# Kernel tuning notes

Hardware: AMD Instinct MI355X
Metric: run time of the kernel (lower is better)

Reference implementation:

```python
import jax, jax.numpy as jnp
import numpy as np

B = 16384
IN_FEATURES = 256
OUT_FEATURES = 4096
CH_GROUP = 8
NUM_SLICE = IN_FEATURES // CH_GROUP  # 32


def setup_inputs() -> dict:
    key = jax.random.key(0)
    kx, kw = jax.random.split(key)
    x = jax.random.normal(kx, (B, IN_FEATURES), dtype=jnp.float32)
    # Stacked weights of the 32 tiny Linear(ch_group -> out_features, bias=False)
    # layers; W[i] corresponds to fc_i.weight with shape [out_features, ch_group].
    W = jax.random.normal(kw, (NUM_SLICE, OUT_FEATURES, CH_GROUP), dtype=jnp.float32) * (1.0 / np.sqrt(CH_GROUP))
    return {"x": x, "W": W}


def reference(x, W):
    # Equivalent to sum_i fc_i(x[:, i*cg:(i+1)*cg]) = fused block GEMM.
    xs = x.reshape(x.shape[0], NUM_SLICE, CH_GROUP)  # [B, S, C]
    # out[b,o] = sum_{s,c} xs[b,s,c] * W[s,o,c]
    return jnp.einsum('bsc,soc->bo', xs, W)
```

## Files before the change

kernel.cpp:

```cpp
#include <hip/hip_runtime.h>
#include <hip/hip_bf16.h>


typedef __attribute__((ext_vector_type(8)))  __bf16          bf16x8;
typedef __attribute__((ext_vector_type(8)))  unsigned short  ushort8;
typedef __attribute__((ext_vector_type(4)))  float           floatx4;

__device__ __forceinline__ unsigned short f2bf(float f) {
    union { float f; unsigned u; } v; v.f = f;
    unsigned r = v.u + 0x7fffu + ((v.u >> 16) & 1u);
    return (unsigned short)(r >> 16);
}

__global__ __launch_bounds__(256) void prep_kernel(
    const float* __restrict__ x, const float* __restrict__ W,
    unsigned short* __restrict__ xb, unsigned short* __restrict__ wb) {
    const int b = blockIdx.x;
    if (b < 2048) {
        const int t = b * 256 + threadIdx.x;
        const float4* p = (const float4*)x;
        float4 a = p[2 * t], c = p[2 * t + 1];
        ushort8 v;
        v[0] = f2bf(a.x); v[1] = f2bf(a.y); v[2] = f2bf(a.z); v[3] = f2bf(a.w);
        v[4] = f2bf(c.x); v[5] = f2bf(c.y); v[6] = f2bf(c.z); v[7] = f2bf(c.w);
        *(ushort8*)(xb + (size_t)t * 8) = v;
    } else {
        const int t = (b - 2048) * 256 + threadIdx.x;
        const int s = t >> 12;
        const int o = t & 4095;
        const float4* p = (const float4*)(W + (size_t)s * 32768 + (size_t)o * 8);
        float4 a = p[0], c = p[1];
        ushort8 v;
        v[0] = f2bf(a.x); v[1] = f2bf(a.y); v[2] = f2bf(a.z); v[3] = f2bf(a.w);
        v[4] = f2bf(c.x); v[5] = f2bf(c.y); v[6] = f2bf(c.z); v[7] = f2bf(c.w);
        *(ushort8*)(wb + (size_t)o * 256 + (size_t)s * 8) = v;
    }
}

__device__ __forceinline__ void gload_lds16(const unsigned short* g, unsigned short* l) {
    __builtin_amdgcn_global_load_lds(
        (const __attribute__((address_space(1))) unsigned int*)(const void*)g,
        (__attribute__((address_space(3))) unsigned int*)(void*)l,
        16, 0, 0);
}

__global__ __launch_bounds__(256, 4) void gemm_kernel(
    const unsigned short* __restrict__ A,
    const unsigned short* __restrict__ Bt,
    float* __restrict__ C) {
    __shared__ __align__(16) unsigned short lsA[2][128 * 32];
    __shared__ __align__(16) unsigned short lsB[2][128 * 32];

    const int tid  = threadIdx.x;
    const int wave = tid >> 6;
    const int lane = tid & 63;

    const int flat = blockIdx.y * 32 + blockIdx.x;
    const int nid  = (flat & 7) * 512 + (flat >> 3);
    const int bm   = nid >> 5;
    const int bn   = nid & 31;

    const int sr  = tid >> 2;
    const int gch = (tid & 3) ^ ((tid >> 3) & 3);
    const unsigned short* Ag = A  + ((size_t)(bm * 128 + sr)) * 256 + gch * 8;
    const unsigned short* Bg = Bt + ((size_t)(bn * 128 + sr)) * 256 + gch * 8;
    unsigned short* laW[2] = { &lsA[0][wave * 512], &lsA[1][wave * 512] };
    unsigned short* lbW[2] = { &lsB[0][wave * 512], &lsB[1][wave * 512] };

    const int wrow = wave >> 1, wcol = wave & 1;
    const int fr = lane & 15;
    const int fq = lane >> 4;
    const int so = (fq ^ ((fr >> 1) & 3)) * 8;
    const unsigned short* aF[2] = { &lsA[0][(wrow * 64 + fr) * 32] + so,
                                    &lsA[1][(wrow * 64 + fr) * 32] + so };
    const unsigned short* bF[2] = { &lsB[0][(wcol * 64 + fr) * 32] + so,
                                    &lsB[1][(wcol * 64 + fr) * 32] + so };

    floatx4 acc[4][4] = {};

    gload_lds16(Ag,            laW[0]);
    gload_lds16(Ag + 64 * 256, laW[0] + 2048);
    gload_lds16(Bg,            lbW[0]);
    gload_lds16(Bg + 64 * 256, lbW[0] + 2048);
    __syncthreads();

#pragma unroll
    for (int kt = 0; kt < 8; ++kt) {
        const int cur = kt & 1;
        if (kt < 7) {
            const int ko = (kt + 1) * 32;
            gload_lds16(Ag + ko,            laW[cur ^ 1]);
            gload_lds16(Ag + ko + 64 * 256, laW[cur ^ 1] + 2048);
            gload_lds16(Bg + ko,            lbW[cur ^ 1]);
            gload_lds16(Bg + ko + 64 * 256, lbW[cur ^ 1] + 2048);
        }

        bf16x8 af[4], bv[4];
#pragma unroll
        for (int i = 0; i < 4; ++i) {
            af[i] = *(const bf16x8*)(const void*)(aF[cur] + i * 512);
            bv[i] = *(const bf16x8*)(const void*)(bF[cur] + i * 512);
        }
#pragma unroll
        for (int j = 0; j < 4; ++j)
#pragma unroll
            for (int i = 0; i < 4; ++i)
                acc[j][i] = __builtin_amdgcn_mfma_f32_16x16x32_bf16(
                    bv[j], af[i], acc[j][i], 0, 0, 0);
        __syncthreads();
    }

    const int row0 = bm * 128 + wrow * 64 + fr;
    const int col0 = bn * 128 + wcol * 64 + fq * 4;
#pragma unroll
    for (int i = 0; i < 4; ++i) {
        float* Cp = C + (size_t)(row0 + i * 16) * 4096 + col0;
#pragma unroll
        for (int j = 0; j < 4; ++j)
            __builtin_nontemporal_store(acc[j][i], (floatx4*)(Cp + j * 16));
    }
}

extern "C" void kernel_launch(void* const* d_in, const int* in_sizes, int n_in,
                              void* d_out, int out_size, void* d_ws, size_t ws_size,
                              hipStream_t stream) {
    const float* x = (const float*)d_in[0];
    const float* W = (const float*)d_in[1];
    float* out = (float*)d_out;

    unsigned short* xb = (unsigned short*)d_ws;
    unsigned short* wb = xb + (size_t)16384 * 256;

    prep_kernel<<<2560, 256, 0, stream>>>(x, W, xb, wb);

    dim3 grid(32, 128);
    gemm_kernel<<<grid, 256, 0, stream>>>(xb, wb, out);
}
```

Baseline: 312.7 us.

## Fuse fp32-to-bf16 conversion into GEMM and drop separate prep kernel

New measurement: 352.8 us. 12.8% more time.

```diff
diff --git a/kernel.cpp b/kernel.cpp
--- a/kernel.cpp
+++ b/kernel.cpp
@@ -2,54 +2,16 @@
 #include <hip/hip_bf16.h>
 
 
-typedef __attribute__((ext_vector_type(8)))  __bf16          bf16x8;
-typedef __attribute__((ext_vector_type(8)))  unsigned short  ushort8;
-typedef __attribute__((ext_vector_type(4)))  float           floatx4;
+typedef __attribute__((ext_vector_type(8))) __bf16 bf16x8;
+typedef __attribute__((ext_vector_type(4))) __bf16 bf16x4;
+typedef __attribute__((ext_vector_type(4))) float  floatx4;
 
-__device__ __forceinline__ unsigned short f2bf(float f) {
-    union { float f; unsigned u; } v; v.f = f;
-    unsigned r = v.u + 0x7fffu + ((v.u >> 16) & 1u);
-    return (unsigned short)(r >> 16);
-}
-
-__global__ __launch_bounds__(256) void prep_kernel(
-    const float* __restrict__ x, const float* __restrict__ W,
-    unsigned short* __restrict__ xb, unsigned short* __restrict__ wb) {
-    const int b = blockIdx.x;
-    if (b < 2048) {
-        const int t = b * 256 + threadIdx.x;
-        const float4* p = (const float4*)x;
-        float4 a = p[2 * t], c = p[2 * t + 1];
-        ushort8 v;
-        v[0] = f2bf(a.x); v[1] = f2bf(a.y); v[2] = f2bf(a.z); v[3] = f2bf(a.w);
-        v[4] = f2bf(c.x); v[5] = f2bf(c.y); v[6] = f2bf(c.z); v[7] = f2bf(c.w);
-        *(ushort8*)(xb + (size_t)t * 8) = v;
-    } else {
-        const int t = (b - 2048) * 256 + threadIdx.x;
-        const int s = t >> 12;
-        const int o = t & 4095;
-        const float4* p = (const float4*)(W + (size_t)s * 32768 + (size_t)o * 8);
-        float4 a = p[0], c = p[1];
-        ushort8 v;
-        v[0] = f2bf(a.x); v[1] = f2bf(a.y); v[2] = f2bf(a.z); v[3] = f2bf(a.w);
-        v[4] = f2bf(c.x); v[5] = f2bf(c.y); v[6] = f2bf(c.z); v[7] = f2bf(c.w);
-        *(ushort8*)(wb + (size_t)o * 256 + (size_t)s * 8) = v;
-    }
-}
-
-__device__ __forceinline__ void gload_lds16(const unsigned short* g, unsigned short* l) {
-    __builtin_amdgcn_global_load_lds(
-        (const __attribute__((address_space(1))) unsigned int*)(const void*)g,
-        (__attribute__((address_space(3))) unsigned int*)(void*)l,
-        16, 0, 0);
-}
-
-__global__ __launch_bounds__(256, 4) void gemm_kernel(
-    const unsigned short* __restrict__ A,
-    const unsigned short* __restrict__ Bt,
+__global__ __launch_bounds__(256) void gemm_kernel(
+    const float* __restrict__ X,
+    const float* __restrict__ W,
     float* __restrict__ C) {
-    __shared__ __align__(16) unsigned short lsA[2][128 * 32];
-    __shared__ __align__(16) unsigned short lsB[2][128 * 32];
+    __shared__ __align__(16) __bf16 lsA[2][128 * 32];
+    __shared__ __align__(16) __bf16 lsB[2][128 * 32];
 
     const int tid  = threadIdx.x;
     const int wave = tid >> 6;
@@ -60,46 +22,58 @@
     const int bm   = nid >> 5;
     const int bn   = nid & 31;
 
-    const int sr  = tid >> 2;
-    const int gch = (tid & 3) ^ ((tid >> 3) & 3);
-    const unsigned short* Ag = A  + ((size_t)(bm * 128 + sr)) * 256 + gch * 8;
-    const unsigned short* Bg = Bt + ((size_t)(bn * 128 + sr)) * 256 + gch * 8;
-    unsigned short* laW[2] = { &lsA[0][wave * 512], &lsA[1][wave * 512] };
-    unsigned short* lbW[2] = { &lsB[0][wave * 512], &lsB[1][wave * 512] };
+    const int achunk = tid & 7;
+    const int arb    = tid >> 3;
+    const int akey   = (arb >> 1) & 3;
+    const float* Xa  = X + (size_t)(bm * 128 + arb) * 256 + achunk * 4;
+    const int adst   = arb * 32 + (((achunk >> 1) ^ akey) * 8) + (achunk & 1) * 4;
+
+    const int brb   = tid >> 1;
+    const int bhalf = tid & 1;
+    const int bkey  = (brb >> 1) & 3;
+    const float* Wb = W + (size_t)(bn * 128 + brb) * 8 + bhalf * 4;
+    const int bdst  = brb * 32 + bhalf * 4;
 
     const int wrow = wave >> 1, wcol = wave & 1;
     const int fr = lane & 15;
     const int fq = lane >> 4;
-    const int so = (fq ^ ((fr >> 1) & 3)) * 8;
-    const unsigned short* aF[2] = { &lsA[0][(wrow * 64 + fr) * 32] + so,
-                                    &lsA[1][(wrow * 64 + fr) * 32] + so };
-    const unsigned short* bF[2] = { &lsB[0][(wcol * 64 + fr) * 32] + so,
-                                    &lsB[1][(wcol * 64 + fr) * 32] + so };
+    const int fch  = (fq ^ ((fr >> 1) & 3)) * 8;
+    const int aoff = (wrow * 64 + fr) * 32 + fch;
+    const int boff = (wcol * 64 + fr) * 32 + fch;
 
+    floatx4 ra[2][4], rb[2][4];
     floatx4 acc[4][4] = {};
 
-    gload_lds16(Ag,            laW[0]);
-    gload_lds16(Ag + 64 * 256, laW[0] + 2048);
-    gload_lds16(Bg,            lbW[0]);
-    gload_lds16(Bg + 64 * 256, lbW[0] + 2048);
-    __syncthreads();
-
+    auto loadT = [&](int set, int kt) {
 #pragma unroll
-    for (int kt = 0; kt < 8; ++kt) {
-        const int cur = kt & 1;
-        if (kt < 7) {
-            const int ko = (kt + 1) * 32;
-            gload_lds16(Ag + ko,            laW[cur ^ 1]);
-            gload_lds16(Ag + ko + 64 * 256, laW[cur ^ 1] + 2048);
-            gload_lds16(Bg + ko,            lbW[cur ^ 1]);
-            gload_lds16(Bg + ko + 64 * 256, lbW[cur ^ 1] + 2048);
+        for (int q = 0; q < 4; ++q)
+            ra[set][q] = *(const floatx4*)(Xa + (size_t)q * 32 * 256 + kt * 32);
+#pragma unroll
+        for (int l = 0; l < 4; ++l)
+            rb[set][l] = *(const floatx4*)(Wb + (size_t)(kt * 4 + l) * 32768);
+    };
+    auto writeT = [&](int buf, int set) {
+#pragma unroll
+        for (int q = 0; q < 4; ++q) {
+            bf16x4 v;
+            v[0] = (__bf16)ra[set][q][0]; v[1] = (__bf16)ra[set][q][1];
+            v[2] = (__bf16)ra[set][q][2]; v[3] = (__bf16)ra[set][q][3];
+            *(bf16x4*)&lsA[buf][adst + q * 1024] = v;
         }
-
+#pragma unroll
+        for (int l = 0; l < 4; ++l) {
+            bf16x4 v;
+            v[0] = (__bf16)rb[set][l][0]; v[1] = (__bf16)rb[set][l][1];
+            v[2] = (__bf16)rb[set][l][2]; v[3] = (__bf16)rb[set][l][3];
+            *(bf16x4*)&lsB[buf][bdst + ((l ^ bkey) * 8)] = v;
+        }
+    };
+    auto compute = [&](int buf) {
         bf16x8 af[4], bv[4];
 #pragma unroll
         for (int i = 0; i < 4; ++i) {
-            af[i] = *(const bf16x8*)(const void*)(aF[cur] + i * 512);
-            bv[i] = *(const bf16x8*)(const void*)(bF[cur] + i * 512);
+            af[i] = *(const bf16x8*)&lsA[buf][aoff + i * 512];
+            bv[i] = *(const bf16x8*)&lsB[buf][boff + i * 512];
         }
 #pragma unroll
         for (int j = 0; j < 4; ++j)
@@ -107,7 +81,24 @@
             for (int i = 0; i < 4; ++i)
                 acc[j][i] = __builtin_amdgcn_mfma_f32_16x16x32_bf16(
                     bv[j], af[i], acc[j][i], 0, 0, 0);
-        __syncthreads();
+    };
+
+    loadT(0, 0);
+    writeT(0, 0);
+    loadT(1, 1);
+    asm volatile("s_waitcnt lgkmcnt(0)" ::: "memory");
+    __builtin_amdgcn_s_barrier();
+
+#pragma unroll
+    for (int kt = 0; kt < 8; ++kt) {
+        const int cur = kt & 1;
+        if (kt < 7) writeT(cur ^ 1, (kt + 1) & 1);
+        if (kt < 6) loadT(cur, kt + 2);
+        compute(cur);
+        if (kt < 7) {
+            asm volatile("s_waitcnt lgkmcnt(0)" ::: "memory");
+            __builtin_amdgcn_s_barrier();
+        }
     }
 
     const int row0 = bm * 128 + wrow * 64 + fr;
@@ -127,12 +118,8 @@
     const float* x = (const float*)d_in[0];
     const float* W = (const float*)d_in[1];
     float* out = (float*)d_out;
-
-    unsigned short* xb = (unsigned short*)d_ws;
-    unsigned short* wb = xb + (size_t)16384 * 256;
-
-    prep_kernel<<<2560, 256, 0, stream>>>(x, W, xb, wb);
+    (void)d_ws; (void)ws_size;
 
     dim3 grid(32, 128);
-    gemm_kernel<<<grid, 256, 0, stream>>>(xb, wb, out);
+    gemm_kernel<<<grid, 256, 0, stream>>>(x, W, out);
 }
```

## Triple-buffer LDS tiles with one barrier per k-step in GEMM

Applied to the files above, without the earlier changes.

After: 305.5 us. 1.02x faster.

```diff
diff --git a/kernel.cpp b/kernel.cpp
--- a/kernel.cpp
+++ b/kernel.cpp
@@ -44,12 +44,18 @@
         16, 0, 0);
 }
 
-__global__ __launch_bounds__(256, 4) void gemm_kernel(
+__device__ __forceinline__ void block_sync() {
+    asm volatile("" ::: "memory");
+    __builtin_amdgcn_s_barrier();
+    asm volatile("" ::: "memory");
+}
+
+__global__ __launch_bounds__(256, 3) void gemm_kernel(
     const unsigned short* __restrict__ A,
     const unsigned short* __restrict__ Bt,
     float* __restrict__ C) {
-    __shared__ __align__(16) unsigned short lsA[2][128 * 32];
-    __shared__ __align__(16) unsigned short lsB[2][128 * 32];
+    __shared__ __align__(16) unsigned short lsA[3][128 * 32];
+    __shared__ __align__(16) unsigned short lsB[3][128 * 32];
 
     const int tid  = threadIdx.x;
     const int wave = tid >> 6;
@@ -64,50 +70,53 @@
     const int gch = (tid & 3) ^ ((tid >> 3) & 3);
     const unsigned short* Ag = A  + ((size_t)(bm * 128 + sr)) * 256 + gch * 8;
     const unsigned short* Bg = Bt + ((size_t)(bn * 128 + sr)) * 256 + gch * 8;
-    unsigned short* laW[2] = { &lsA[0][wave * 512], &lsA[1][wave * 512] };
-    unsigned short* lbW[2] = { &lsB[0][wave * 512], &lsB[1][wave * 512] };
+    unsigned short* laW[3] = { &lsA[0][wave * 512], &lsA[1][wave * 512], &lsA[2][wave * 512] };
+    unsigned short* lbW[3] = { &lsB[0][wave * 512], &lsB[1][wave * 512], &lsB[2][wave * 512] };
 
     const int wrow = wave >> 1, wcol = wave & 1;
     const int fr = lane & 15;
     const int fq = lane >> 4;
     const int so = (fq ^ ((fr >> 1) & 3)) * 8;
-    const unsigned short* aF[2] = { &lsA[0][(wrow * 64 + fr) * 32] + so,
-                                    &lsA[1][(wrow * 64 + fr) * 32] + so };
-    const unsigned short* bF[2] = { &lsB[0][(wcol * 64 + fr) * 32] + so,
-                                    &lsB[1][(wcol * 64 + fr) * 32] + so };
+    const unsigned short* aF[3] = { &lsA[0][(wrow * 64 + fr) * 32] + so,
+                                    &lsA[1][(wrow * 64 + fr) * 32] + so,
+                                    &lsA[2][(wrow * 64 + fr) * 32] + so };
+    const unsigned short* bF[3] = { &lsB[0][(wcol * 64 + fr) * 32] + so,
+                                    &lsB[1][(wcol * 64 + fr) * 32] + so,
+                                    &lsB[2][(wcol * 64 + fr) * 32] + so };
 
     floatx4 acc[4][4] = {};
 
-    gload_lds16(Ag,            laW[0]);
-    gload_lds16(Ag + 64 * 256, laW[0] + 2048);
-    gload_lds16(Bg,            lbW[0]);
-    gload_lds16(Bg + 64 * 256, lbW[0] + 2048);
-    __syncthreads();
+    auto stage = [&](int b, int kt) {
+        const int ko = kt * 32;
+        gload_lds16(Ag + ko,            laW[b]);
+        gload_lds16(Ag + ko + 64 * 256, laW[b] + 2048);
+        gload_lds16(Bg + ko,            lbW[b]);
+        gload_lds16(Bg + ko + 64 * 256, lbW[b] + 2048);
+    };
+
+    stage(0, 0);
+    stage(1, 1);
 
 #pragma unroll
     for (int kt = 0; kt < 8; ++kt) {
-        const int cur = kt & 1;
-        if (kt < 7) {
-            const int ko = (kt + 1) * 32;
-            gload_lds16(Ag + ko,            laW[cur ^ 1]);
-            gload_lds16(Ag + ko + 64 * 256, laW[cur ^ 1] + 2048);
-            gload_lds16(Bg + ko,            lbW[cur ^ 1]);
-            gload_lds16(Bg + ko + 64 * 256, lbW[cur ^ 1] + 2048);
-        }
+        const int b = kt % 3;
+        if (kt < 7) asm volatile("s_waitcnt vmcnt(4)" ::: "memory");
+        else        asm volatile("s_waitcnt vmcnt(0)" ::: "memory");
+        block_sync();
 
         bf16x8 af[4], bv[4];
 #pragma unroll
         for (int i = 0; i < 4; ++i) {
-            af[i] = *(const bf16x8*)(const void*)(aF[cur] + i * 512);
-            bv[i] = *(const bf16x8*)(const void*)(bF[cur] + i * 512);
+            af[i] = *(const bf16x8*)(const void*)(aF[b] + i * 512);
+            bv[i] = *(const bf16x8*)(const void*)(bF[b] + i * 512);
         }
+        if (kt < 6) stage((kt + 2) % 3, kt + 2);
 #pragma unroll
         for (int j = 0; j < 4; ++j)
 #pragma unroll
             for (int i = 0; i < 4; ++i)
                 acc[j][i] = __builtin_amdgcn_mfma_f32_16x16x32_bf16(
                     bv[j], af[i], acc[j][i], 0, 0, 0);
-        __syncthreads();
     }
 
     const int row0 = bm * 128 + wrow * 64 + fr;
```
